# Optimization experiments

Measured on AMD Instinct MI355X. Metric: run time of the kernel, lower is better.

Reference implementation:

```python
import jax, jax.numpy as jnp
import numpy as np

D_MODEL = 1024
H = 16
D_K = D_MODEL // H
BAND = 100  # attention allowed where |i-j| < BAND


def setup_inputs() -> dict:
    key = jax.random.key(0)
    ks = jax.random.split(key, 9)
    B, S = 2, 2048
    s = 1.0 / np.sqrt(D_MODEL)
    return {
        "x": jax.random.normal(ks[0], (B, S, D_MODEL), jnp.float32),
        "Wq": jax.random.normal(ks[1], (D_MODEL, D_MODEL), jnp.float32) * s,
        "bq": jnp.zeros((D_MODEL,), jnp.float32),
        "Wk": jax.random.normal(ks[2], (D_MODEL, D_MODEL), jnp.float32) * s,
        "bk": jnp.zeros((D_MODEL,), jnp.float32),
        "Wv": jax.random.normal(ks[3], (D_MODEL, D_MODEL), jnp.float32) * s,
        "bv": jnp.zeros((D_MODEL,), jnp.float32),
        "Wo": jax.random.normal(ks[4], (D_MODEL, D_MODEL), jnp.float32) * s,
        "bo": jnp.zeros((D_MODEL,), jnp.float32),
    }


def _split_heads(t, B, S):
    # [B, S, D] -> [B, H, S, D_K]
    return t.reshape(B, S, H, D_K).transpose(0, 2, 1, 3)


def reference(x, Wq, bq, Wk, bk, Wv, bv, Wo, bo):
    B, S, _ = x.shape
    q = _split_heads(x @ Wq.T + bq, B, S)
    k = _split_heads(x @ Wk.T + bk, B, S)
    v = _split_heads(x @ Wv.T + bv, B, S)

    scores = jnp.einsum("bhqd,bhkd->bhqk", q, k) / jnp.sqrt(jnp.float32(D_K))
    i = jnp.arange(S)
    band = jnp.abs(i[:, None] - i[None, :]) < BAND  # [S, S] True inside band
    scores = jnp.where(band[None, None, :, :], scores, jnp.float32(-1e9))
    p_attn = jax.nn.softmax(scores, axis=-1)

    out = jnp.einsum("bhqk,bhkd->bhqd", p_attn, v)
    out = out.transpose(0, 2, 1, 3).reshape(B, S, D_MODEL)
    return out @ Wo.T + bo
```

## Files before the change

kernel.cpp:

```cpp
#include <hip/hip_runtime.h>
#include <hip/hip_bf16.h>


typedef __attribute__((ext_vector_type(8))) short short8;
typedef __attribute__((ext_vector_type(4))) float f32x4;

#define S_LEN 2048
#define NH 16
#define DK 64
#define BANDW 100

#define X_ELEMS   (2 * S_LEN * 1024)
#define W_ELEMS   (1024 * 1024)
#define QKV_ELEMS (2 * NH * S_LEN * DK)
#define AO_ELEMS  (2 * S_LEN * 1024)

__device__ __attribute__((aligned(256))) short g_X[X_ELEMS];
__device__ __attribute__((aligned(256))) short g_W[4 * W_ELEMS];
__device__ __attribute__((aligned(256))) short g_b[4 * 1024];
__device__ __attribute__((aligned(256))) short g_Q[QKV_ELEMS];
__device__ __attribute__((aligned(256))) short g_K[QKV_ELEMS];
__device__ __attribute__((aligned(256))) short g_V[QKV_ELEMS];
__device__ __attribute__((aligned(256))) short g_AO[AO_ELEMS];

__device__ __forceinline__ float bf2f(short u) {
    unsigned x = ((unsigned)(unsigned short)u) << 16;
    return __builtin_bit_cast(float, x);
}
__device__ __forceinline__ short f2bf(float f) {
    unsigned x = __builtin_bit_cast(unsigned, f);
    unsigned r = (x + 0x7fffu + ((x >> 16) & 1u)) >> 16;
    return (short)r;
}

#define GLOAD_LDS(gp, lp) \
    __builtin_amdgcn_global_load_lds( \
        (const __attribute__((address_space(1))) void*)(gp), \
        (__attribute__((address_space(3))) void*)(lp), 16, 0, 0)

#define XC   (X_ELEMS / 8)
#define WC   (W_ELEMS / 8)
#define BC   (1024 / 8)
#define TOTC (XC + 4 * WC + 4 * BC)

__global__ __launch_bounds__(256) void convert_all(
    const void* __restrict__ x,
    const void* __restrict__ w0, const void* __restrict__ b0,
    const void* __restrict__ w1, const void* __restrict__ b1,
    const void* __restrict__ w2, const void* __restrict__ b2,
    const void* __restrict__ w3, const void* __restrict__ b3)
{
    __shared__ int cnt[256];
    {
        const unsigned* xw = (const unsigned*)x;
        int local = 0;
        #pragma unroll
        for (int i = 0; i < 4; i++) {
            unsigned wv = xw[threadIdx.x * 4 + i];
            unsigned e = (wv >> 7) & 0xFF;
            if (e >= 100 && e <= 140) local++;
        }
        cnt[threadIdx.x] = local;
    }
    __syncthreads();
    for (int s = 128; s > 0; s >>= 1) {
        if (threadIdx.x < s) cnt[threadIdx.x] += cnt[threadIdx.x + s];
        __syncthreads();
    }
    const int is_bf16 = (cnt[0] > 512);

    long i = (long)blockIdx.x * 256 + threadIdx.x;
    if (i >= TOTC) return;

    const void* src; short* dst; long off;
    if (i < XC)                { src = x;  dst = g_X;              off = i; }
    else if ((i -= XC) < WC)   { src = w0; dst = g_W + 0L*W_ELEMS; off = i; }
    else if ((i -= WC) < WC)   { src = w1; dst = g_W + 1L*W_ELEMS; off = i; }
    else if ((i -= WC) < WC)   { src = w2; dst = g_W + 2L*W_ELEMS; off = i; }
    else if ((i -= WC) < WC)   { src = w3; dst = g_W + 3L*W_ELEMS; off = i; }
    else if ((i -= WC) < BC)   { src = b0; dst = g_b + 0*1024;     off = i; }
    else if ((i -= BC) < BC)   { src = b1; dst = g_b + 1*1024;     off = i; }
    else if ((i -= BC) < BC)   { src = b2; dst = g_b + 2*1024;     off = i; }
    else                       { src = b3; dst = g_b + 3*1024;     off = i - BC; }

    if (is_bf16) {
        ((short8*)dst)[off] = ((const short8*)src)[off];
    } else {
        const float* s = (const float*)src + off * 8;
        short8 o;
        #pragma unroll
        for (int e = 0; e < 8; e++) o[e] = f2bf(s[e]);
        ((short8*)dst)[off] = o;
    }
}

__global__ __launch_bounds__(256) void qkv_gemm()
{
    __shared__ __attribute__((aligned(16))) short As[128 * 32];
    __shared__ __attribute__((aligned(16))) short Bs[128 * 32];

    const int z = blockIdx.z;
    const short* __restrict__ X = g_X;
    const short* __restrict__ W = g_W + (long)z * W_ELEMS;
    const short* __restrict__ bias = g_b + z * 1024;
    short* __restrict__ Out = (z == 0) ? g_Q : ((z == 1) ? g_K : g_V);

    const int t = threadIdx.x;
    const int lane = t & 63;
    const int wid  = t >> 6;
    const int wm = wid & 1, wn = wid >> 1;
    const int l15 = lane & 15;
    const int q8  = (lane >> 4) * 8;
    const int mb = blockIdx.x * 128;
    const int nb = blockIdx.y * 128;

    const long ga0 = (long)(mb + (t >> 2)) * 1024 + (t & 3) * 8;
    const long ga1 = (long)(mb + 64 + (t >> 2)) * 1024 + (t & 3) * 8;
    const long gb0 = (long)(nb + (t >> 2)) * 1024 + (t & 3) * 8;
    const long gb1 = (long)(nb + 64 + (t >> 2)) * 1024 + (t & 3) * 8;
    short* lA0 = As + t * 8;
    short* lA1 = As + 2048 + t * 8;
    short* lB0 = Bs + t * 8;
    short* lB1 = Bs + 2048 + t * 8;

    f32x4 acc[4][4] = {};

    for (int k0 = 0; k0 < 1024; k0 += 32) {
        __syncthreads();
        GLOAD_LDS(X + ga0 + k0, lA0);
        GLOAD_LDS(X + ga1 + k0, lA1);
        GLOAD_LDS(W + gb0 + k0, lB0);
        GLOAD_LDS(W + gb1 + k0, lB1);
        __syncthreads();

        short8 a[4], b[4];
        #pragma unroll
        for (int mt = 0; mt < 4; mt++) a[mt] = *(const short8*)(As + (wm * 64 + mt * 16 + l15) * 32 + q8);
        #pragma unroll
        for (int nt = 0; nt < 4; nt++) b[nt] = *(const short8*)(Bs + (wn * 64 + nt * 16 + l15) * 32 + q8);
        #pragma unroll
        for (int mt = 0; mt < 4; mt++)
            #pragma unroll
            for (int nt = 0; nt < 4; nt++)
                acc[mt][nt] = __builtin_amdgcn_mfma_f32_16x16x32_bf16(a[mt], b[nt], acc[mt][nt], 0, 0, 0);
    }

    const int rg = (lane >> 4) * 4;
    #pragma unroll
    for (int nt = 0; nt < 4; nt++) {
        const int col = nb + wn * 64 + nt * 16 + l15;
        const float bv_ = bf2f(bias[col]);
        const int h = col >> 6, d = col & 63;
        #pragma unroll
        for (int mt = 0; mt < 4; mt++) {
            #pragma unroll
            for (int r = 0; r < 4; r++) {
                const int row = mb + wm * 64 + mt * 16 + rg + r;
                const int bI = row >> 11, s = row & 2047;
                Out[(((long)(bI * NH + h) * S_LEN) + s) * DK + d] = f2bf(acc[mt][nt][r] + bv_);
            }
        }
    }
}

__global__ __launch_bounds__(256) void o_gemm(float* __restrict__ Out)
{
    __shared__ __attribute__((aligned(16))) short As[128 * 32];
    __shared__ __attribute__((aligned(16))) short Bs[64 * 32];

    const short* __restrict__ A = g_AO;
    const short* __restrict__ W = g_W + 3L * W_ELEMS;

    const int t = threadIdx.x;
    const int lane = t & 63;
    const int wid  = t >> 6;
    const int wm = wid & 1, wn = wid >> 1;
    const int l15 = lane & 15;
    const int q8  = (lane >> 4) * 8;
    const int mb = blockIdx.x * 128;
    const int nb = blockIdx.y * 64;

    const long ga0 = (long)(mb + (t >> 2)) * 1024 + (t & 3) * 8;
    const long ga1 = (long)(mb + 64 + (t >> 2)) * 1024 + (t & 3) * 8;
    const long gb0 = (long)(nb + (t >> 2)) * 1024 + (t & 3) * 8;
    short* lA0 = As + t * 8;
    short* lA1 = As + 2048 + t * 8;
    short* lB0 = Bs + t * 8;

    f32x4 acc[4][2] = {};

    for (int k0 = 0; k0 < 1024; k0 += 32) {
        __syncthreads();
        GLOAD_LDS(A + ga0 + k0, lA0);
        GLOAD_LDS(A + ga1 + k0, lA1);
        GLOAD_LDS(W + gb0 + k0, lB0);
        __syncthreads();

        short8 a[4], b[2];
        #pragma unroll
        for (int mt = 0; mt < 4; mt++) a[mt] = *(const short8*)(As + (wm * 64 + mt * 16 + l15) * 32 + q8);
        #pragma unroll
        for (int nt = 0; nt < 2; nt++) b[nt] = *(const short8*)(Bs + (wn * 32 + nt * 16 + l15) * 32 + q8);
        #pragma unroll
        for (int mt = 0; mt < 4; mt++)
            #pragma unroll
            for (int nt = 0; nt < 2; nt++)
                acc[mt][nt] = __builtin_amdgcn_mfma_f32_16x16x32_bf16(a[mt], b[nt], acc[mt][nt], 0, 0, 0);
    }

    const int rg = (lane >> 4) * 4;
    #pragma unroll
    for (int nt = 0; nt < 2; nt++) {
        const int col = nb + wn * 32 + nt * 16 + l15;
        const float bv_ = bf2f(g_b[3 * 1024 + col]);
        #pragma unroll
        for (int mt = 0; mt < 4; mt++) {
            #pragma unroll
            for (int r = 0; r < 4; r++) {
                const int row = mb + wm * 64 + mt * 16 + rg + r;
                Out[(long)row * 1024 + col] = acc[mt][nt][r] + bv_;
            }
        }
    }
}

#define VT_PAD 328

__global__ __launch_bounds__(256) void attn_kernel()
{
    __shared__ __attribute__((aligned(16))) short Vt[64][VT_PAD];
    __shared__ __attribute__((aligned(16))) short Pl[4][16][72];

    const int bid = blockIdx.x;
    const int qt = bid & 31;
    const int h  = (bid >> 5) & 15;
    const int b  = bid >> 9;
    const int qbase = qt * 64;

    const int lane = threadIdx.x & 63;
    const int w    = threadIdx.x >> 6;
    const int l15  = lane & 15;
    const int qg   = lane >> 4;
    const int q8   = qg * 8;

    const long hoff = (long)(b * NH + h) * S_LEN * DK;
    const short* __restrict__ Qh = g_Q + hoff;
    const short* __restrict__ Kh = g_K + hoff;
    const short* __restrict__ Vh = g_V + hoff;

    const int lo  = qbase - (BANDW - 1);
    const int kc0 = (lo < 0 ? 0 : lo) >> 6;
    int hi = qbase + 64 + (BANDW - 1);
    if (hi > S_LEN) hi = S_LEN;
    const int kc1 = (hi + 63) >> 6;
    const int kb0 = kc0 * 64;
    const int n_keys = (kc1 - kc0) * 64;

    const short* qp = Qh + (long)(qbase + w * 16 + l15) * DK + q8;
    const short8 aq0 = *(const short8*)(qp);
    const short8 aq1 = *(const short8*)(qp + 32);

    for (int kk = threadIdx.x; kk < n_keys; kk += 256) {
        const short* vp = Vh + (long)(kb0 + kk) * DK;
        #pragma unroll
        for (int tq = 0; tq < 8; tq++) {
            const short8 v = *(const short8*)(vp + tq * 8);
            #pragma unroll
            for (int e = 0; e < 8; e++) Vt[tq * 8 + e][kk] = v[e];
        }
    }
    __syncthreads();

    f32x4 o[4] = {};
    float m_r[4], l_r[4];
    #pragma unroll
    for (int r = 0; r < 4; r++) { m_r[r] = -1e30f; l_r[r] = 0.f; }

    for (int kc = kc0; kc < kc1; kc++) {
        const int kb = kc * 64;
        const int kloc = kb - kb0;

        f32x4 sc[4];
        #pragma unroll
        for (int nt = 0; nt < 4; nt++) {
            const short* kp = Kh + (long)(kb + nt * 16 + l15) * DK + q8;
            const short8 bk0 = *(const short8*)(kp);
            const short8 bk1 = *(const short8*)(kp + 32);
            f32x4 z = {};
            z = __builtin_amdgcn_mfma_f32_16x16x32_bf16(aq0, bk0, z, 0, 0, 0);
            z = __builtin_amdgcn_mfma_f32_16x16x32_bf16(aq1, bk1, z, 0, 0, 0);
            sc[nt] = z;
        }

        float pv[4][4];
        float mx[4] = {-1e30f, -1e30f, -1e30f, -1e30f};
        #pragma unroll
        for (int nt = 0; nt < 4; nt++) {
            const int kg = kb + nt * 16 + l15;
            #pragma unroll
            for (int r = 0; r < 4; r++) {
                const int qI = qbase + w * 16 + qg * 4 + r;
                int dlt = qI - kg; if (dlt < 0) dlt = -dlt;
                const float v = (dlt < BANDW) ? sc[nt][r] * 0.125f : -1e30f;
                pv[nt][r] = v;
                mx[r] = fmaxf(mx[r], v);
            }
        }
        #pragma unroll
        for (int mk = 1; mk < 16; mk <<= 1)
            #pragma unroll
            for (int r = 0; r < 4; r++) mx[r] = fmaxf(mx[r], __shfl_xor(mx[r], mk, 64));

        float alpha[4], lnew[4];
        #pragma unroll
        for (int r = 0; r < 4; r++) {
            const float mn = fmaxf(m_r[r], mx[r]);
            alpha[r] = __builtin_exp2f((m_r[r] - mn) * 1.44269504f);
            m_r[r] = mn;
            lnew[r] = 0.f;
        }
        #pragma unroll
        for (int nt = 0; nt < 4; nt++)
            #pragma unroll
            for (int r = 0; r < 4; r++) {
                const float p = (pv[nt][r] > -0.5e30f)
                    ? __builtin_exp2f((pv[nt][r] - m_r[r]) * 1.44269504f) : 0.f;
                pv[nt][r] = p;
                lnew[r] += p;
            }
        #pragma unroll
        for (int mk = 1; mk < 16; mk <<= 1)
            #pragma unroll
            for (int r = 0; r < 4; r++) lnew[r] += __shfl_xor(lnew[r], mk, 64);
        #pragma unroll
        for (int r = 0; r < 4; r++) l_r[r] = l_r[r] * alpha[r] + lnew[r];
        #pragma unroll
        for (int nt2 = 0; nt2 < 4; nt2++)
            #pragma unroll
            for (int r = 0; r < 4; r++) o[nt2][r] *= alpha[r];

        #pragma unroll
        for (int nt = 0; nt < 4; nt++)
            #pragma unroll
            for (int r = 0; r < 4; r++)
                Pl[w][qg * 4 + r][nt * 16 + l15] = f2bf(pv[nt][r]);
        asm volatile("s_waitcnt lgkmcnt(0)" ::: "memory");
        const short8 ap0 = *(const short8*)(&Pl[w][l15][q8]);
        const short8 ap1 = *(const short8*)(&Pl[w][l15][32 + q8]);

        #pragma unroll
        for (int nt2 = 0; nt2 < 4; nt2++) {
            const short* vrow = &Vt[nt2 * 16 + l15][kloc];
            const short8 bv0 = *(const short8*)(vrow + q8);
            const short8 bv1 = *(const short8*)(vrow + 32 + q8);
            o[nt2] = __builtin_amdgcn_mfma_f32_16x16x32_bf16(ap0, bv0, o[nt2], 0, 0, 0);
            o[nt2] = __builtin_amdgcn_mfma_f32_16x16x32_bf16(ap1, bv1, o[nt2], 0, 0, 0);
        }
    }

    #pragma unroll
    for (int nt2 = 0; nt2 < 4; nt2++)
        #pragma unroll
        for (int r = 0; r < 4; r++) {
            const int qI = qbase + w * 16 + qg * 4 + r;
            const int d = nt2 * 16 + l15;
            g_AO[((long)b * S_LEN + qI) * 1024 + h * DK + d] = f2bf(o[nt2][r] / l_r[r]);
        }
}

extern "C" void kernel_launch(void* const* d_in, const int* in_sizes, int n_in,
                              void* d_out, int out_size, void* d_ws, size_t ws_size,
                              hipStream_t stream) {
    float* out = (float*)d_out;

    convert_all<<<(TOTC + 255) / 256, 256, 0, stream>>>(
        d_in[0], d_in[1], d_in[2], d_in[3], d_in[4], d_in[5], d_in[6], d_in[7], d_in[8]);
    qkv_gemm<<<dim3(32, 8, 3), 256, 0, stream>>>();
    attn_kernel<<<dim3(2 * NH * (S_LEN / 64)), 256, 0, stream>>>();
    o_gemm<<<dim3(32, 16), 256, 0, stream>>>(out);
}
```

Before: 179.0 us.

## Double GEMM K-tile with XOR-swizzled LDS and use single-pass softmax in attention

Both GEMMs now stage a K-step of 64 instead of 32 per barrier pair, with an XOR swizzle on the LDS chunk index to avoid bank conflicts on MFMA operand reads. This halves the loop trip count and the number of syncthreads. The attention kernel changes block ordering so heads vary fastest, and packs pairs of keys into 32-bit LDS writes for the V transpose. It also replaces the online softmax with a two-pass scheme: all up-to-five key chunks of scores are held in registers, then the max and sum are reduced once. This raises register pressure and LDS use.

```diff
diff --git a/kernel.cpp b/kernel.cpp
--- a/kernel.cpp
+++ b/kernel.cpp
@@ -96,8 +96,8 @@
 
 __global__ __launch_bounds__(256) void qkv_gemm()
 {
-    __shared__ __attribute__((aligned(16))) short As[128 * 32];
-    __shared__ __attribute__((aligned(16))) short Bs[128 * 32];
+    __shared__ __attribute__((aligned(16))) short As[128 * 64];
+    __shared__ __attribute__((aligned(16))) short Bs[128 * 64];
 
     const int z = blockIdx.z;
     const short* __restrict__ X = g_X;
@@ -110,42 +110,55 @@
     const int wid  = t >> 6;
     const int wm = wid & 1, wn = wid >> 1;
     const int l15 = lane & 15;
-    const int q8  = (lane >> 4) * 8;
+    const int g   = lane >> 4;
     const int mb = blockIdx.x * 128;
     const int nb = blockIdx.y * 128;
 
-    const long ga0 = (long)(mb + (t >> 2)) * 1024 + (t & 3) * 8;
-    const long ga1 = (long)(mb + 64 + (t >> 2)) * 1024 + (t & 3) * 8;
-    const long gb0 = (long)(nb + (t >> 2)) * 1024 + (t & 3) * 8;
-    const long gb1 = (long)(nb + 64 + (t >> 2)) * 1024 + (t & 3) * 8;
-    short* lA0 = As + t * 8;
-    short* lA1 = As + 2048 + t * 8;
-    short* lB0 = Bs + t * 8;
-    short* lB1 = Bs + 2048 + t * 8;
+    long gA[4], gB[4];
+    #pragma unroll
+    for (int i = 0; i < 4; i++) {
+        const int R = i * 32 + (t >> 3);
+        const int l = (t & 7) ^ (R & 7);
+        gA[i] = (long)(mb + R) * 1024 + l * 8;
+        gB[i] = (long)(nb + R) * 1024 + l * 8;
+    }
+    short* lA = As + t * 8;
+    short* lB = Bs + t * 8;
 
     f32x4 acc[4][4] = {};
 
-    for (int k0 = 0; k0 < 1024; k0 += 32) {
+    for (int k0 = 0; k0 < 1024; k0 += 64) {
         __syncthreads();
-        GLOAD_LDS(X + ga0 + k0, lA0);
-        GLOAD_LDS(X + ga1 + k0, lA1);
-        GLOAD_LDS(W + gb0 + k0, lB0);
-        GLOAD_LDS(W + gb1 + k0, lB1);
+        #pragma unroll
+        for (int i = 0; i < 4; i++) GLOAD_LDS(X + gA[i] + k0, lA + i * 2048);
+        #pragma unroll
+        for (int i = 0; i < 4; i++) GLOAD_LDS(W + gB[i] + k0, lB + i * 2048);
         __syncthreads();
 
-        short8 a[4], b[4];
-        #pragma unroll
-        for (int mt = 0; mt < 4; mt++) a[mt] = *(const short8*)(As + (wm * 64 + mt * 16 + l15) * 32 + q8);
-        #pragma unroll
-        for (int nt = 0; nt < 4; nt++) b[nt] = *(const short8*)(Bs + (wn * 64 + nt * 16 + l15) * 32 + q8);
-        #pragma unroll
-        for (int mt = 0; mt < 4; mt++)
-            #pragma unroll
-            for (int nt = 0; nt < 4; nt++)
-                acc[mt][nt] = __builtin_amdgcn_mfma_f32_16x16x32_bf16(a[mt], b[nt], acc[mt][nt], 0, 0, 0);
-    }
-
-    const int rg = (lane >> 4) * 4;
+        #pragma unroll
+        for (int kh = 0; kh < 2; kh++) {
+            short8 a[4], b[4];
+            #pragma unroll
+            for (int mt = 0; mt < 4; mt++) {
+                const int r = wm * 64 + mt * 16 + l15;
+                const int phys = (g + kh * 4) ^ (r & 7);
+                a[mt] = *(const short8*)(As + r * 64 + phys * 8);
+            }
+            #pragma unroll
+            for (int nt = 0; nt < 4; nt++) {
+                const int r = wn * 64 + nt * 16 + l15;
+                const int phys = (g + kh * 4) ^ (r & 7);
+                b[nt] = *(const short8*)(Bs + r * 64 + phys * 8);
+            }
+            #pragma unroll
+            for (int mt = 0; mt < 4; mt++)
+                #pragma unroll
+                for (int nt = 0; nt < 4; nt++)
+                    acc[mt][nt] = __builtin_amdgcn_mfma_f32_16x16x32_bf16(a[mt], b[nt], acc[mt][nt], 0, 0, 0);
+        }
+    }
+
+    const int rg = g * 4;
     #pragma unroll
     for (int nt = 0; nt < 4; nt++) {
         const int col = nb + wn * 64 + nt * 16 + l15;
@@ -165,8 +178,8 @@
 
 __global__ __launch_bounds__(256) void o_gemm(float* __restrict__ Out)
 {
-    __shared__ __attribute__((aligned(16))) short As[128 * 32];
-    __shared__ __attribute__((aligned(16))) short Bs[64 * 32];
+    __shared__ __attribute__((aligned(16))) short As[128 * 64];
+    __shared__ __attribute__((aligned(16))) short Bs[64 * 64];
 
     const short* __restrict__ A = g_AO;
     const short* __restrict__ W = g_W + 3L * W_ELEMS;
@@ -176,39 +189,60 @@
     const int wid  = t >> 6;
     const int wm = wid & 1, wn = wid >> 1;
     const int l15 = lane & 15;
-    const int q8  = (lane >> 4) * 8;
+    const int g   = lane >> 4;
     const int mb = blockIdx.x * 128;
     const int nb = blockIdx.y * 64;
 
-    const long ga0 = (long)(mb + (t >> 2)) * 1024 + (t & 3) * 8;
-    const long ga1 = (long)(mb + 64 + (t >> 2)) * 1024 + (t & 3) * 8;
-    const long gb0 = (long)(nb + (t >> 2)) * 1024 + (t & 3) * 8;
-    short* lA0 = As + t * 8;
-    short* lA1 = As + 2048 + t * 8;
-    short* lB0 = Bs + t * 8;
+    long gA[4], gB[2];
+    #pragma unroll
+    for (int i = 0; i < 4; i++) {
+        const int R = i * 32 + (t >> 3);
+        const int l = (t & 7) ^ (R & 7);
+        gA[i] = (long)(mb + R) * 1024 + l * 8;
+    }
+    #pragma unroll
+    for (int i = 0; i < 2; i++) {
+        const int R = i * 32 + (t >> 3);
+        const int l = (t & 7) ^ (R & 7);
+        gB[i] = (long)(nb + R) * 1024 + l * 8;
+    }
+    short* lA = As + t * 8;
+    short* lB = Bs + t * 8;
 
     f32x4 acc[4][2] = {};
 
-    for (int k0 = 0; k0 < 1024; k0 += 32) {
+    for (int k0 = 0; k0 < 1024; k0 += 64) {
         __syncthreads();
-        GLOAD_LDS(A + ga0 + k0, lA0);
-        GLOAD_LDS(A + ga1 + k0, lA1);
-        GLOAD_LDS(W + gb0 + k0, lB0);
+        #pragma unroll
+        for (int i = 0; i < 4; i++) GLOAD_LDS(A + gA[i] + k0, lA + i * 2048);
+        #pragma unroll
+        for (int i = 0; i < 2; i++) GLOAD_LDS(W + gB[i] + k0, lB + i * 2048);
         __syncthreads();
 
-        short8 a[4], b[2];
-        #pragma unroll
-        for (int mt = 0; mt < 4; mt++) a[mt] = *(const short8*)(As + (wm * 64 + mt * 16 + l15) * 32 + q8);
-        #pragma unroll
-        for (int nt = 0; nt < 2; nt++) b[nt] = *(const short8*)(Bs + (wn * 32 + nt * 16 + l15) * 32 + q8);
-        #pragma unroll
-        for (int mt = 0; mt < 4; mt++)
-            #pragma unroll
-            for (int nt = 0; nt < 2; nt++)
-                acc[mt][nt] = __builtin_amdgcn_mfma_f32_16x16x32_bf16(a[mt], b[nt], acc[mt][nt], 0, 0, 0);
-    }
-
-    const int rg = (lane >> 4) * 4;
+        #pragma unroll
+        for (int kh = 0; kh < 2; kh++) {
+            short8 a[4], b[2];
+            #pragma unroll
+            for (int mt = 0; mt < 4; mt++) {
+                const int r = wm * 64 + mt * 16 + l15;
+                const int phys = (g + kh * 4) ^ (r & 7);
+                a[mt] = *(const short8*)(As + r * 64 + phys * 8);
+            }
+            #pragma unroll
+            for (int nt = 0; nt < 2; nt++) {
+                const int r = wn * 32 + nt * 16 + l15;
+                const int phys = (g + kh * 4) ^ (r & 7);
+                b[nt] = *(const short8*)(Bs + r * 64 + phys * 8);
+            }
+            #pragma unroll
+            for (int mt = 0; mt < 4; mt++)
+                #pragma unroll
+                for (int nt = 0; nt < 2; nt++)
+                    acc[mt][nt] = __builtin_amdgcn_mfma_f32_16x16x32_bf16(a[mt], b[nt], acc[mt][nt], 0, 0, 0);
+        }
+    }
+
+    const int rg = g * 4;
     #pragma unroll
     for (int nt = 0; nt < 2; nt++) {
         const int col = nb + wn * 32 + nt * 16 + l15;
@@ -231,10 +265,10 @@
     __shared__ __attribute__((aligned(16))) short Vt[64][VT_PAD];
     __shared__ __attribute__((aligned(16))) short Pl[4][16][72];
 
-    const int bid = blockIdx.x;
-    const int qt = bid & 31;
-    const int h  = (bid >> 5) & 15;
-    const int b  = bid >> 9;
+    const int bid  = blockIdx.x;
+    const int head = bid & 31;
+    const int qt   = bid >> 5;
+    const int h = head & 15, b = head >> 4;
     const int qbase = qt * 64;
 
     const int lane = threadIdx.x & 63;
@@ -254,33 +288,35 @@
     if (hi > S_LEN) hi = S_LEN;
     const int kc1 = (hi + 63) >> 6;
     const int kb0 = kc0 * 64;
-    const int n_keys = (kc1 - kc0) * 64;
+    const int nkc = kc1 - kc0;
+    const int n_keys = nkc * 64;
 
     const short* qp = Qh + (long)(qbase + w * 16 + l15) * DK + q8;
     const short8 aq0 = *(const short8*)(qp);
     const short8 aq1 = *(const short8*)(qp + 32);
 
-    for (int kk = threadIdx.x; kk < n_keys; kk += 256) {
-        const short* vp = Vh + (long)(kb0 + kk) * DK;
+    const int npairs = n_keys >> 1;
+    for (int u = threadIdx.x; u < npairs; u += 256) {
+        const short* vp0 = Vh + (long)(kb0 + 2 * u) * DK;
         #pragma unroll
         for (int tq = 0; tq < 8; tq++) {
-            const short8 v = *(const short8*)(vp + tq * 8);
-            #pragma unroll
-            for (int e = 0; e < 8; e++) Vt[tq * 8 + e][kk] = v[e];
+            const short8 v0 = *(const short8*)(vp0 + tq * 8);
+            const short8 v1 = *(const short8*)(vp0 + DK + tq * 8);
+            #pragma unroll
+            for (int e = 0; e < 8; e++) {
+                const int pk = (int)(unsigned short)v0[e] | ((int)(unsigned short)v1[e] << 16);
+                *(int*)&Vt[tq * 8 + e][2 * u] = pk;
+            }
         }
     }
     __syncthreads();
 
-    f32x4 o[4] = {};
-    float m_r[4], l_r[4];
-    #pragma unroll
-    for (int r = 0; r < 4; r++) { m_r[r] = -1e30f; l_r[r] = 0.f; }
-
-    for (int kc = kc0; kc < kc1; kc++) {
-        const int kb = kc * 64;
-        const int kloc = kb - kb0;
-
-        f32x4 sc[4];
+    f32x4 sc[5][4];
+    float mx[4] = {-1e30f, -1e30f, -1e30f, -1e30f};
+    #pragma unroll
+    for (int c = 0; c < 5; c++) {
+        const bool live = (c < nkc);
+        const int kb = kb0 + (live ? c : 0) * 64;
         #pragma unroll
         for (int nt = 0; nt < 4; nt++) {
             const short* kp = Kh + (long)(kb + nt * 16 + l15) * DK + q8;
@@ -289,61 +325,49 @@
             f32x4 z = {};
             z = __builtin_amdgcn_mfma_f32_16x16x32_bf16(aq0, bk0, z, 0, 0, 0);
             z = __builtin_amdgcn_mfma_f32_16x16x32_bf16(aq1, bk1, z, 0, 0, 0);
-            sc[nt] = z;
-        }
-
-        float pv[4][4];
-        float mx[4] = {-1e30f, -1e30f, -1e30f, -1e30f};
-        #pragma unroll
-        for (int nt = 0; nt < 4; nt++) {
             const int kg = kb + nt * 16 + l15;
             #pragma unroll
             for (int r = 0; r < 4; r++) {
                 const int qI = qbase + w * 16 + qg * 4 + r;
                 int dlt = qI - kg; if (dlt < 0) dlt = -dlt;
-                const float v = (dlt < BANDW) ? sc[nt][r] * 0.125f : -1e30f;
-                pv[nt][r] = v;
+                const float v = (live && dlt < BANDW) ? z[r] * 0.125f : -1e30f;
+                sc[c][nt][r] = v;
                 mx[r] = fmaxf(mx[r], v);
             }
         }
-        #pragma unroll
-        for (int mk = 1; mk < 16; mk <<= 1)
-            #pragma unroll
-            for (int r = 0; r < 4; r++) mx[r] = fmaxf(mx[r], __shfl_xor(mx[r], mk, 64));
-
-        float alpha[4], lnew[4];
-        #pragma unroll
-        for (int r = 0; r < 4; r++) {
-            const float mn = fmaxf(m_r[r], mx[r]);
-            alpha[r] = __builtin_exp2f((m_r[r] - mn) * 1.44269504f);
-            m_r[r] = mn;
-            lnew[r] = 0.f;
-        }
+    }
+    #pragma unroll
+    for (int mk = 1; mk < 16; mk <<= 1)
+        #pragma unroll
+        for (int r = 0; r < 4; r++) mx[r] = fmaxf(mx[r], __shfl_xor(mx[r], mk, 64));
+
+    float lsum[4] = {0.f, 0.f, 0.f, 0.f};
+    #pragma unroll
+    for (int c = 0; c < 5; c++)
         #pragma unroll
         for (int nt = 0; nt < 4; nt++)
             #pragma unroll
             for (int r = 0; r < 4; r++) {
-                const float p = (pv[nt][r] > -0.5e30f)
-                    ? __builtin_exp2f((pv[nt][r] - m_r[r]) * 1.44269504f) : 0.f;
-                pv[nt][r] = p;
-                lnew[r] += p;
-            }
-        #pragma unroll
-        for (int mk = 1; mk < 16; mk <<= 1)
-            #pragma unroll
-            for (int r = 0; r < 4; r++) lnew[r] += __shfl_xor(lnew[r], mk, 64);
-        #pragma unroll
-        for (int r = 0; r < 4; r++) l_r[r] = l_r[r] * alpha[r] + lnew[r];
-        #pragma unroll
-        for (int nt2 = 0; nt2 < 4; nt2++)
-            #pragma unroll
-            for (int r = 0; r < 4; r++) o[nt2][r] *= alpha[r];
-
+                const float p = (sc[c][nt][r] > -0.5e30f)
+                    ? __builtin_exp2f((sc[c][nt][r] - mx[r]) * 1.44269504f) : 0.f;
+                sc[c][nt][r] = p;
+                lsum[r] += p;
+            }
+    #pragma unroll
+    for (int mk = 1; mk < 16; mk <<= 1)
+        #pragma unroll
+        for (int r = 0; r < 4; r++) lsum[r] += __shfl_xor(lsum[r], mk, 64);
+
+    f32x4 o[4] = {};
+    #pragma unroll
+    for (int c = 0; c < 5; c++) {
+        if (c >= nkc) break;
+        const int kloc = c * 64;
         #pragma unroll
         for (int nt = 0; nt < 4; nt++)
             #pragma unroll
             for (int r = 0; r < 4; r++)
-                Pl[w][qg * 4 + r][nt * 16 + l15] = f2bf(pv[nt][r]);
+                Pl[w][qg * 4 + r][nt * 16 + l15] = f2bf(sc[c][nt][r]);
         asm volatile("s_waitcnt lgkmcnt(0)" ::: "memory");
         const short8 ap0 = *(const short8*)(&Pl[w][l15][q8]);
         const short8 ap1 = *(const short8*)(&Pl[w][l15][32 + q8]);
@@ -364,7 +388,7 @@
         for (int r = 0; r < 4; r++) {
             const int qI = qbase + w * 16 + qg * 4 + r;
             const int d = nt2 * 16 + l15;
-            g_AO[((long)b * S_LEN + qI) * 1024 + h * DK + d] = f2bf(o[nt2][r] / l_r[r]);
+            g_AO[((long)b * S_LEN + qI) * 1024 + h * DK + d] = f2bf(o[nt2][r] / lsum[r]);
         }
 }
 
```

Result: slower. 184.2 us (+2.9%).

## Fold softmax scale into Q, prefetch K tiles, pack V transpose, reorder blocks

Applied to the files above, without the earlier changes.

Several independent changes land together. The 1/sqrt(dk) scale is folded into the Q projection epilogue, and the band-mask check is skipped on the diagonal key chunk. K fragments for the next chunk are prefetched into registers, V is transposed into LDS two keys at a time with 32-bit stores, and the block index is remapped so neighbouring blocks cover different heads at the same query tile. The aims are to hide K load latency, halve the LDS store count and cut per-element ALU work, at the cost of extra register pressure and scaling Q before bf16 rounding.

```diff
diff --git a/kernel.cpp b/kernel.cpp
--- a/kernel.cpp
+++ b/kernel.cpp
@@ -104,6 +104,7 @@
     const short* __restrict__ W = g_W + (long)z * W_ELEMS;
     const short* __restrict__ bias = g_b + z * 1024;
     short* __restrict__ Out = (z == 0) ? g_Q : ((z == 1) ? g_K : g_V);
+    const float scale = (z == 0) ? 0.125f : 1.0f;
 
     const int t = threadIdx.x;
     const int lane = t & 63;
@@ -157,7 +158,7 @@
             for (int r = 0; r < 4; r++) {
                 const int row = mb + wm * 64 + mt * 16 + rg + r;
                 const int bI = row >> 11, s = row & 2047;
-                Out[(((long)(bI * NH + h) * S_LEN) + s) * DK + d] = f2bf(acc[mt][nt][r] + bv_);
+                Out[(((long)(bI * NH + h) * S_LEN) + s) * DK + d] = f2bf((acc[mt][nt][r] + bv_) * scale);
             }
         }
     }
@@ -231,10 +232,10 @@
     __shared__ __attribute__((aligned(16))) short Vt[64][VT_PAD];
     __shared__ __attribute__((aligned(16))) short Pl[4][16][72];
 
-    const int bid = blockIdx.x;
-    const int qt = bid & 31;
-    const int h  = (bid >> 5) & 15;
-    const int b  = bid >> 9;
+    const int bid  = blockIdx.x;
+    const int head = bid & 31;
+    const int qt   = bid >> 5;
+    const int h = head & 15, b = head >> 4;
     const int qbase = qt * 64;
 
     const int lane = threadIdx.x & 63;
@@ -260,16 +261,29 @@
     const short8 aq0 = *(const short8*)(qp);
     const short8 aq1 = *(const short8*)(qp + 32);
 
-    for (int kk = threadIdx.x; kk < n_keys; kk += 256) {
-        const short* vp = Vh + (long)(kb0 + kk) * DK;
+    const int npairs = n_keys >> 1;
+    for (int u = threadIdx.x; u < npairs; u += 256) {
+        const short* vp0 = Vh + (long)(kb0 + 2 * u) * DK;
         #pragma unroll
         for (int tq = 0; tq < 8; tq++) {
-            const short8 v = *(const short8*)(vp + tq * 8);
-            #pragma unroll
-            for (int e = 0; e < 8; e++) Vt[tq * 8 + e][kk] = v[e];
+            const short8 v0 = *(const short8*)(vp0 + tq * 8);
+            const short8 v1 = *(const short8*)(vp0 + DK + tq * 8);
+            #pragma unroll
+            for (int e = 0; e < 8; e++) {
+                const int pk = (int)(unsigned short)v0[e] | ((int)(unsigned short)v1[e] << 16);
+                *(int*)&Vt[tq * 8 + e][2 * u] = pk;
+            }
         }
     }
     __syncthreads();
+
+    short8 nk0[4], nk1[4];
+    #pragma unroll
+    for (int nt = 0; nt < 4; nt++) {
+        const short* kp = Kh + (long)(kb0 + nt * 16 + l15) * DK + q8;
+        nk0[nt] = *(const short8*)(kp);
+        nk1[nt] = *(const short8*)(kp + 32);
+    }
 
     f32x4 o[4] = {};
     float m_r[4], l_r[4];
@@ -280,30 +294,50 @@
         const int kb = kc * 64;
         const int kloc = kb - kb0;
 
+        short8 bk0[4], bk1[4];
+        #pragma unroll
+        for (int nt = 0; nt < 4; nt++) { bk0[nt] = nk0[nt]; bk1[nt] = nk1[nt]; }
+        if (kc + 1 < kc1) {
+            const int kbn = kb + 64;
+            #pragma unroll
+            for (int nt = 0; nt < 4; nt++) {
+                const short* kp = Kh + (long)(kbn + nt * 16 + l15) * DK + q8;
+                nk0[nt] = *(const short8*)(kp);
+                nk1[nt] = *(const short8*)(kp + 32);
+            }
+        }
+
         f32x4 sc[4];
         #pragma unroll
         for (int nt = 0; nt < 4; nt++) {
-            const short* kp = Kh + (long)(kb + nt * 16 + l15) * DK + q8;
-            const short8 bk0 = *(const short8*)(kp);
-            const short8 bk1 = *(const short8*)(kp + 32);
             f32x4 z = {};
-            z = __builtin_amdgcn_mfma_f32_16x16x32_bf16(aq0, bk0, z, 0, 0, 0);
-            z = __builtin_amdgcn_mfma_f32_16x16x32_bf16(aq1, bk1, z, 0, 0, 0);
+            z = __builtin_amdgcn_mfma_f32_16x16x32_bf16(aq0, bk0[nt], z, 0, 0, 0);
+            z = __builtin_amdgcn_mfma_f32_16x16x32_bf16(aq1, bk1[nt], z, 0, 0, 0);
             sc[nt] = z;
         }
 
         float pv[4][4];
         float mx[4] = {-1e30f, -1e30f, -1e30f, -1e30f};
-        #pragma unroll
-        for (int nt = 0; nt < 4; nt++) {
-            const int kg = kb + nt * 16 + l15;
-            #pragma unroll
-            for (int r = 0; r < 4; r++) {
-                const int qI = qbase + w * 16 + qg * 4 + r;
-                int dlt = qI - kg; if (dlt < 0) dlt = -dlt;
-                const float v = (dlt < BANDW) ? sc[nt][r] * 0.125f : -1e30f;
-                pv[nt][r] = v;
-                mx[r] = fmaxf(mx[r], v);
+        if (kb == qbase) {
+            #pragma unroll
+            for (int nt = 0; nt < 4; nt++)
+                #pragma unroll
+                for (int r = 0; r < 4; r++) {
+                    pv[nt][r] = sc[nt][r];
+                    mx[r] = fmaxf(mx[r], sc[nt][r]);
+                }
+        } else {
+            #pragma unroll
+            for (int nt = 0; nt < 4; nt++) {
+                const int kg = kb + nt * 16 + l15;
+                #pragma unroll
+                for (int r = 0; r < 4; r++) {
+                    const int qI = qbase + w * 16 + qg * 4 + r;
+                    int dlt = qI - kg; if (dlt < 0) dlt = -dlt;
+                    const float v = (dlt < BANDW) ? sc[nt][r] : -1e30f;
+                    pv[nt][r] = v;
+                    mx[r] = fmaxf(mx[r], v);
+                }
             }
         }
         #pragma unroll
```

After: 175.7 us. Within noise of the previous version (-1.8%).
